# Optimization experiments

Hardware: AMD Instinct MI355X
Metric: run time of the kernel (lower is better)

The kernel has to match this reference:

```python
import jax, jax.numpy as jnp
import numpy as np

T, B, I, H, L, TAPE = 512, 1, 1024, 1024, 2, 30


def setup_inputs() -> dict:
    key = jax.random.key(0)
    ks = jax.random.split(key, 9)
    s = 1.0 / np.sqrt(H)  # pytorch LSTM default init scale
    u = lambda k, sh: jax.random.uniform(k, sh, jnp.float32, -s, s)
    return {
        "xs": jax.random.normal(ks[0], (T, B, I), jnp.float32),
        "w_ih": u(ks[1], (L, 4 * H, I)),
        "w_hh": u(ks[2], (L, 4 * H, H)),
        "b_ih": u(ks[3], (L, 4 * H)),
        "b_hh": u(ks[4], (L, 4 * H)),
        "attn_wh": jax.random.normal(ks[5], (L, H, H), jnp.float32),
        "attn_wx": jax.random.normal(ks[6], (L, H, I), jnp.float32),
        "attn_wht": jax.random.normal(ks[7], (L, H, H), jnp.float32),
        "attn_v": jax.random.normal(ks[8], (L, H), jnp.float32),
    }


def _lstm_step(x, h_prev, c_prev, w_ih, w_hh, b_ih, b_hh):
    # x: (B, I); h_prev, c_prev: (L, B, H). PyTorch gate order i,f,g,o. No dropout (eval/deterministic).
    inp = x
    hs, cs = [], []
    for l in range(L):
        g = inp @ w_ih[l].T + b_ih[l] + h_prev[l] @ w_hh[l].T + b_hh[l]
        i_g, f_g, g_g, o_g = jnp.split(g, 4, axis=-1)
        c = jax.nn.sigmoid(f_g) * c_prev[l] + jax.nn.sigmoid(i_g) * jnp.tanh(g_g)
        h = jax.nn.sigmoid(o_g) * jnp.tanh(c)
        hs.append(h)
        cs.append(c)
        inp = h
    return jnp.stack(hs), jnp.stack(cs)  # (L, B, H) each


def _forward(xs, w_ih, w_hh, b_ih, b_hh, attn_wh, attn_wx, attn_wht, attn_v):
    zeros_state = jnp.zeros((L, B, H), xs.dtype)

    # Phase 1: prev_hidden/cell tapes are never updated in the first loop, so each of the
    # first TAPE steps runs the LSTM from a zero state -> fully parallel via vmap.
    p1 = lambda x: _lstm_step(x, zeros_state, zeros_state, w_ih, w_hh, b_ih, b_hh)
    h1, c1 = jax.vmap(p1)(xs[:TAPE])  # (TAPE, L, B, H)
    h_tape = jax.lax.stop_gradient(h1)  # .detach() in the original
    c_tape = jax.lax.stop_gradient(c1)

    cum = jnp.zeros((T, H), xs.dtype)
    cum = cum.at[:TAPE].set(h1[:, -1, 0, :])  # hidden_state[-1].squeeze(), B==1

    # einsum('jll,...') / einsum('ijj,...') only use the diagonals of attn_wh / attn_wht
    diag_wh = jnp.diagonal(attn_wh, axis1=1, axis2=2)    # (L, H)
    diag_wht = jnp.diagonal(attn_wht, axis1=1, axis2=2)  # (L, H)

    def step(carry, x):
        h_tape, c_tape, prev_h = carry
        hidden_attn = diag_wh[None, :, None, :] * h_tape          # (TAPE, L, B, H)
        x_attn = jnp.einsum('lhi,bi->lbh', attn_wx, x)            # (L, B, H)
        ht_attn = diag_wht[:, None, :] * prev_h                   # (L, B, H)
        a = jnp.tanh(hidden_attn + (x_attn + ht_attn)[None])      # (TAPE, L, B, H)
        scores = jnp.einsum('tlbh,lh->tlb', a, attn_v)            # (TAPE, L, B)
        alpha = jax.nn.softmax(scores, axis=0)                    # softmax over tape dim
        new_h = jnp.einsum('tlb,tlbh->lbh', alpha, h_tape)
        new_c = jnp.einsum('tlb,tlbh->lbh', alpha, c_tape)
        h, c = _lstm_step(x, new_h, new_c, w_ih, w_hh, b_ih, b_hh)
        h_tape = jnp.concatenate([h_tape[1:], h[None]], axis=0)   # tape shift
        c_tape = jnp.concatenate([c_tape[1:], c[None]], axis=0)
        return (h_tape, c_tape, new_h), h[-1, 0, :]

    _, ys = jax.lax.scan(step, (h_tape, c_tape, zeros_state), xs[TAPE:])
    # second loop indexes cum from 0, overwriting the phase-1 entries (faithful to source)
    cum = cum.at[: T - TAPE].set(ys)
    return cum


def reference(xs, w_ih, w_hh, b_ih, b_hh, attn_wh, attn_wx, attn_wht, attn_v):
    return _forward(xs, w_ih, w_hh, b_ih, b_hh, attn_wh, attn_wx, attn_wht, attn_v)
```

## Files before the change

kernel.cpp:

```cpp
#include <hip/hip_runtime.h>
#include <math.h>

#define LSTRIDE 4194304

__device__ __forceinline__ float sigf(float x) { return 1.0f / (1.0f + expf(-x)); }

__device__ __forceinline__ float cload(const float* p) {
  return __hip_atomic_load(p, __ATOMIC_RELAXED, __HIP_MEMORY_SCOPE_AGENT);
}
__device__ __forceinline__ void cstore(float* p, float v) {
  __hip_atomic_store(p, v, __ATOMIC_RELAXED, __HIP_MEMORY_SCOPE_AGENT);
}
__device__ __forceinline__ float2 cload2(const float* p) {
  unsigned long long v = __hip_atomic_load((const unsigned long long*)p,
                                           __ATOMIC_RELAXED, __HIP_MEMORY_SCOPE_AGENT);
  float2 r;
  r.x = __uint_as_float((unsigned)v);
  r.y = __uint_as_float((unsigned)(v >> 32));
  return r;
}
__device__ __forceinline__ void cstore2(float* p, float2 v) {
  unsigned long long u = ((unsigned long long)__float_as_uint(v.y) << 32) |
                         (unsigned long long)__float_as_uint(v.x);
  __hip_atomic_store((unsigned long long*)p, u, __ATOMIC_RELAXED, __HIP_MEMORY_SCOPE_AGENT);
}

__global__ __launch_bounds__(256) void gemm_nt(
    const float* __restrict__ A, const float* __restrict__ X, float* __restrict__ Out,
    const float* __restrict__ b1, const float* __restrict__ b2,
    int M, int ldx, int ldo)
{
  __shared__ float As[64][65];
  __shared__ float Xs[64][65];
  const int tid = threadIdx.x;
  const int tn = tid & 15, tm = tid >> 4;
  const int bn = blockIdx.x * 64, bm = blockIdx.y * 64;
  float acc[4][4];
  #pragma unroll
  for (int i = 0; i < 4; ++i)
    #pragma unroll
    for (int j = 0; j < 4; ++j) acc[i][j] = 0.f;

  for (int k0 = 0; k0 < 1024; k0 += 64) {
    #pragma unroll
    for (int r = 0; r < 4; ++r) {
      int linear = r * 1024 + tid * 4;
      int nn = linear >> 6, kk = linear & 63;
      float4 av = *(const float4*)(A + (size_t)(bn + nn) * 1024 + k0 + kk);
      As[nn][kk+0] = av.x; As[nn][kk+1] = av.y; As[nn][kk+2] = av.z; As[nn][kk+3] = av.w;
      float4 xv = make_float4(0.f, 0.f, 0.f, 0.f);
      if (bm + nn < M) xv = *(const float4*)(X + (size_t)(bm + nn) * ldx + k0 + kk);
      Xs[nn][kk+0] = xv.x; Xs[nn][kk+1] = xv.y; Xs[nn][kk+2] = xv.z; Xs[nn][kk+3] = xv.w;
    }
    __syncthreads();
    #pragma unroll 16
    for (int kk = 0; kk < 64; ++kk) {
      float av[4], xv[4];
      #pragma unroll
      for (int u = 0; u < 4; ++u) { av[u] = As[tn*4+u][kk]; xv[u] = Xs[tm*4+u][kk]; }
      #pragma unroll
      for (int i = 0; i < 4; ++i)
        #pragma unroll
        for (int j = 0; j < 4; ++j) acc[i][j] += xv[i] * av[j];
    }
    __syncthreads();
  }
  #pragma unroll
  for (int i = 0; i < 4; ++i) {
    int m = bm + tm * 4 + i;
    if (m >= M) continue;
    #pragma unroll
    for (int j = 0; j < 4; ++j) {
      int n = bn + tn * 4 + j;
      float r = acc[i][j];
      if (b1) r += b1[n];
      if (b2) r += b2[n];
      Out[(size_t)m * ldo + n] = r;
    }
  }
}

__global__ void diag_k(const float* __restrict__ wh, const float* __restrict__ wht,
                       float* __restrict__ diag)
{
  int i = blockIdx.x * 256 + threadIdx.x;
  if (i < 2048) {
    int l = i >> 10, h = i & 1023;
    size_t idx = (size_t)l * 1048576 + (size_t)h * 1025;
    diag[i]        = wh[idx];
    diag[2048 + i] = wht[idx];
  }
}

__global__ __launch_bounds__(256) void phase1_l0_k(const float* __restrict__ XI0,
    float* __restrict__ tapeh, float* __restrict__ tapec, float* __restrict__ h0p1)
{
  int t = blockIdx.x;
  #pragma unroll
  for (int r = 0; r < 4; ++r) {
    int c = threadIdx.x + r * 256;
    float gi = XI0[t*4096 + c];
    float gg = XI0[t*4096 + 2048 + c];
    float go = XI0[t*4096 + 3072 + c];
    float cc = sigf(gi) * tanhf(gg);
    float hh = sigf(go) * tanhf(cc);
    tapeh[t*2048 + c] = hh;
    tapec[t*2048 + c] = cc;
    h0p1[t*1024 + c] = hh;
  }
}

__global__ __launch_bounds__(256) void phase1_l1_k(const float* __restrict__ G1,
    float* __restrict__ tapeh, float* __restrict__ tapec)
{
  int t = blockIdx.x;
  #pragma unroll
  for (int r = 0; r < 4; ++r) {
    int c = threadIdx.x + r * 256;
    float gi = G1[t*4096 + c];
    float gg = G1[t*4096 + 2048 + c];
    float go = G1[t*4096 + 3072 + c];
    float cc = sigf(gi) * tanhf(gg);
    float hh = sigf(go) * tanhf(cc);
    tapeh[t*2048 + 1024 + c] = hh;
    tapec[t*2048 + 1024 + c] = cc;
  }
}

__device__ __forceinline__ float red16(float p) {
  #pragma unroll
  for (int o = 8; o >= 1; o >>= 1) p += __shfl_xor(p, o, 16);
  return p;
}

__device__ __forceinline__ void arrive(unsigned* __restrict__ base, int gw) {
  asm volatile("s_waitcnt vmcnt(0)" ::: "memory");
  __syncthreads();
  if (threadIdx.x == 0) {
    unsigned o = __hip_atomic_fetch_add(&base[(gw >> 3) * 16], 1u,
                                        __ATOMIC_RELAXED, __HIP_MEMORY_SCOPE_AGENT);
    if (((o + 1) & 7u) == 0u) {
      unsigned o2 = __hip_atomic_fetch_add(&base[256], 1u,
                                           __ATOMIC_RELAXED, __HIP_MEMORY_SCOPE_AGENT);
      if (((o2 + 1) & 15u) == 0u)
        __hip_atomic_store(&base[320], (o2 + 1) >> 4,
                           __ATOMIC_RELAXED, __HIP_MEMORY_SCOPE_AGENT);
    }
  }
}

__device__ __forceinline__ void waitf(const unsigned* __restrict__ fOwn, unsigned tOwn,
                                      const unsigned* __restrict__ fOth, unsigned tOth) {
  if (threadIdx.x < 2) {
    const unsigned* fp = threadIdx.x ? fOth : fOwn;
    unsigned tgt = threadIdx.x ? tOth : tOwn;
    if (tgt) {
      while (__hip_atomic_load(fp, __ATOMIC_RELAXED, __HIP_MEMORY_SCOPE_AGENT) < tgt)
        __builtin_amdgcn_s_sleep(1);
    }
  }
  __syncthreads();
  asm volatile("" ::: "memory");
}

template <int LW>
__device__ __forceinline__ void run_group(
    const int gw,
    const float* __restrict__ wih, const float* __restrict__ whh,
    const float* __restrict__ bih, const float* __restrict__ bhh,
    const float* __restrict__ diag, const float* __restrict__ av,
    const float* __restrict__ XI0, const float* __restrict__ XA,
    const float* __restrict__ tapehG, const float* __restrict__ tapecG,
    const float* __restrict__ Pg,
    float* __restrict__ scoresG, float* __restrict__ prevh,
    float* __restrict__ h0cur, float* __restrict__ h1cur,
    float* __restrict__ outp, unsigned* __restrict__ bar,
    float* tape, float* hA, float* hB, float* Pl, float* tc,
    float* sc, float* aw, float* gls, float* ihs, float* ncs,
    float* bsum, float* sred)
{
  const int tid = threadIdx.x;
  const int rid = tid >> 4, sub = tid & 15;
  const int cell = (gw << 3) + (rid & 7);
  const int row = ((rid >> 3) << 10) + cell;
  const bool isScore = (gw < 29);
  const int h2 = tid * 2;

  unsigned* __restrict__ barOwn = bar + (LW ? 512 : 0);
  const unsigned* __restrict__ fOwn = barOwn + 320;
  const unsigned* __restrict__ fOth = bar + (LW ? 0 : 512) + 320;

  float wA[64];
  float wB[LW ? 64 : 1];
  {
    const float* pa = whh + (size_t)LW * LSTRIDE + (size_t)row * 1024 + sub * 64;
    #pragma unroll
    for (int i = 0; i < 16; ++i) {
      float4 v = ((const float4*)pa)[i];
      wA[4*i] = v.x; wA[4*i+1] = v.y; wA[4*i+2] = v.z; wA[4*i+3] = v.w;
    }
    if (LW) {
      const float* pb = wih + LSTRIDE + (size_t)row * 1024 + sub * 64;
      #pragma unroll
      for (int i = 0; i < 16; ++i) {
        float4 v = ((const float4*)pb)[i];
        wB[4*i] = v.x; wB[4*i+1] = v.y; wB[4*i+2] = v.z; wB[4*i+3] = v.w;
      }
    }
  }
  if (LW && sub == 0) bsum[rid] = bih[4096 + row] + bhh[4096 + row];
  for (int k = tid; k < 960; k += 512) {
    int s = k >> 5, r = k & 31;
    int rr = ((r >> 3) << 10) + (gw << 3) + (r & 7);
    Pl[s * 34 + r] = Pg[s * 4096 + rr];
  }
  for (int k = tid; k < 240; k += 512) {
    int s = k >> 3, c = k & 7;
    tc[s * 9 + c] = tapecG[s * 2048 + LW * 1024 + (gw << 3) + c];
  }
  if (isScore) {
    for (int k = tid; k < 7680; k += 512) {
      int s = k >> 8, off = (k & 255) << 2;
      *(float4*)&tape[s * 1024 + off] =
          *(const float4*)&tapehG[s * 2048 + LW * 1024 + off];
    }
  }
  const float ddx = diag[LW*1024 + h2],        ddy = diag[LW*1024 + h2 + 1];
  const float ttx = diag[2048 + LW*1024 + h2], tty = diag[2048 + LW*1024 + h2 + 1];
  const float vvx = av[LW*1024 + h2],          vvy = av[LW*1024 + h2 + 1];
  __syncthreads();

  if (isScore) {
    for (int s = gw; s < 30; s += 29) {
      float2 xa = *(const float2*)&XA[(size_t)30 * 2048 + LW * 1024 + h2];
      float part = vvx * tanhf(ddx * tape[s*1024 + h2] + xa.x)
                 + vvy * tanhf(ddy * tape[s*1024 + h2 + 1] + xa.y);
      #pragma unroll
      for (int o = 32; o >= 1; o >>= 1) part += __shfl_xor(part, o, 64);
      if ((tid & 63) == 0) sred[tid >> 6] = part;
      __syncthreads();
      if (tid == 0) {
        float tot = 0.f;
        #pragma unroll
        for (int i = 0; i < 8; ++i) tot += sred[i];
        cstore(&scoresG[LW * 32 + s], tot);
      }
      __syncthreads();
    }
  }
  arrive(barOwn, gw);

  for (int t = 30; t < 512; ++t) {
    unsigned tOwn = (unsigned)(t - 29);
    unsigned tOth;
    if (LW == 0) tOth = (t >= 33) ? (unsigned)(t - 32) : 0u;
    else         tOth = (unsigned)(t - 28);
    waitf(fOwn, tOwn, fOth, tOth);

    const int tmod = t % 30;
    const int pslot = (tmod == 0) ? 29 : tmod - 1;

    if (tid < 30) sc[tid] = cload(&scoresG[(t & 1) * 64 + LW * 32 + tid]);
    float2 hva, hvb = make_float2(0.f, 0.f), ph = make_float2(0.f, 0.f),
           xan = make_float2(0.f, 0.f);
    if (LW == 0) {
      hva = cload2(&h0cur[(size_t)((t - 1) & 3) * 1024 + h2]);
    } else {
      hva = cload2(&h0cur[(size_t)(t & 3) * 1024 + h2]);
      hvb = cload2(&h1cur[((t - 1) & 1) * 1024 + h2]);
    }
    if (t > 30) {
      ph  = cload2(&prevh[((t - 1) & 1) * 2048 + LW * 1024 + h2]);
      xan = *(const float2*)&XA[(size_t)t * 2048 + LW * 1024 + h2];
    }
    float xi = 0.f;
    if (LW == 0 && sub == 0) xi = XI0[(size_t)t * 4096 + row];
    {
      int o = (h2 >> 6) * 66 + (h2 & 63);
      hA[o] = hva.x; hA[o + 1] = hva.y;
      if (LW) { hB[o] = hvb.x; hB[o + 1] = hvb.y; }
    }
    __syncthreads();

    if (t > 30) {
      float2 hn = LW ? hvb : hva;
      float np = vvx * tanhf(ddx * hn.x + xan.x + ttx * ph.x)
               + vvy * tanhf(ddy * hn.y + xan.y + tty * ph.y);
      #pragma unroll
      for (int o = 32; o >= 1; o >>= 1) np += __shfl_xor(np, o, 64);
      if ((tid & 63) == 0) sred[tid >> 6] = np;
      const float* hbufP = LW ? hB : hA;
      float pc = 0.f;
      #pragma unroll
      for (int i = 0; i < 64; ++i) pc += wA[i] * hbufP[sub * 66 + i];
      pc = red16(pc);
      if (sub == 0) Pl[pslot * 34 + rid] = pc;
      if (isScore) {
        tape[pslot * 1024 + h2]     = hn.x;
        tape[pslot * 1024 + h2 + 1] = hn.y;
      }
    }
    if (LW) {
      float ih = 0.f;
      #pragma unroll
      for (int i = 0; i < 64; ++i) ih += wB[i] * hA[sub * 66 + i];
      ih = red16(ih);
      if (sub == 0) ihs[rid] = ih + bsum[rid];
    }
    __syncthreads();

    if (tid < 32) {
      float npv = 0.f;
      if (t > 30) {
        float x = (tid < 8) ? sred[tid] : 0.f;
        #pragma unroll
        for (int o = 4; o >= 1; o >>= 1) x += __shfl_xor(x, o, 8);
        npv = __shfl(x, 0, 32);
      }
      float v = (tid < 30) ? sc[tid] : -1e30f;
      if (t > 30 && tid == pslot) v = npv;
      float m = v;
      #pragma unroll
      for (int o = 16; o >= 1; o >>= 1) m = fmaxf(m, __shfl_xor(m, o, 32));
      float e = (tid < 30) ? expf(v - m) : 0.f;
      float sm = e;
      #pragma unroll
      for (int o = 16; o >= 1; o >>= 1) sm += __shfl_xor(sm, o, 32);
      aw[tid] = e / sm;
    }
    __syncthreads();

    {
      float p = aw[sub] * Pl[sub * 34 + rid];
      if (sub < 14) p += aw[sub + 16] * Pl[(sub + 16) * 34 + rid];
      p = red16(p);
      if (sub == 0) gls[rid] = p + (LW ? ihs[rid] : xi);
      if (rid < 8) {
        float pn = aw[sub] * tc[sub * 9 + rid];
        if (sub < 14) pn += aw[sub + 16] * tc[(sub + 16) * 9 + rid];
        pn = red16(pn);
        if (sub == 0) ncs[rid] = pn;
      }
    }
    __syncthreads();

    if (tid < 8) {
      float gi = gls[tid], gf = gls[8 + tid], gg = gls[16 + tid], go = gls[24 + tid];
      float cv = sigf(gf) * ncs[tid] + sigf(gi) * tanhf(gg);
      float hv = sigf(go) * tanhf(cv);
      if (LW == 0) {
        cstore(&h0cur[(size_t)(t & 3) * 1024 + (gw << 3) + tid], hv);
      } else {
        outp[(size_t)(t - 30) * 1024 + (gw << 3) + tid] = hv;
        cstore(&h1cur[(t & 1) * 1024 + (gw << 3) + tid], hv);
      }
      tc[tmod * 9 + tid] = cv;
    }

    if (isScore && t < 511) {
      int ss = tmod + 1 + gw; if (ss >= 30) ss -= 30;
      float ax = 0.f, ay = 0.f;
      #pragma unroll
      for (int s = 0; s < 30; ++s) {
        float as = aw[s];
        ax += as * tape[s * 1024 + h2];
        ay += as * tape[s * 1024 + h2 + 1];
      }
      if (gw == 0) cstore2(&prevh[(t & 1) * 2048 + LW * 1024 + h2],
                           make_float2(ax, ay));
      float2 xa2 = *(const float2*)&XA[(size_t)(t + 1) * 2048 + LW * 1024 + h2];
      float part = vvx * tanhf(ddx * tape[ss * 1024 + h2] + xa2.x + ttx * ax)
                 + vvy * tanhf(ddy * tape[ss * 1024 + h2 + 1] + xa2.y + tty * ay);
      #pragma unroll
      for (int o = 32; o >= 1; o >>= 1) part += __shfl_xor(part, o, 64);
      if ((tid & 63) == 0) sred[tid >> 6] = part;
      __syncthreads();
      if (tid == 0) {
        float tot = 0.f;
        #pragma unroll
        for (int i = 0; i < 8; ++i) tot += sred[i];
        cstore(&scoresG[((t + 1) & 1) * 64 + LW * 32 + ss], tot);
      }
    }

    arrive(barOwn, gw);
  }
}

__global__ __launch_bounds__(512, 2) void scan_fused(
    const float* __restrict__ wih, const float* __restrict__ whh,
    const float* __restrict__ bih, const float* __restrict__ bhh,
    const float* __restrict__ diag, const float* __restrict__ av,
    const float* __restrict__ XI0, const float* __restrict__ XA,
    const float* __restrict__ tapehG, const float* __restrict__ tapecG,
    const float* __restrict__ P0g, const float* __restrict__ P1g,
    float* __restrict__ scoresG, float* __restrict__ prevh,
    float* __restrict__ h0cur, float* __restrict__ h1cur,
    float* __restrict__ outp, unsigned* __restrict__ bar)
{
  __shared__ float tape[30 * 1024];
  __shared__ float hA[16 * 66], hB[16 * 66];
  __shared__ float Pl[30 * 34];
  __shared__ float tc[30 * 9];
  __shared__ float sc[32], aw[32], gls[32], ihs[32], ncs[8], bsum[32], sred[8];
  if (blockIdx.x < 128)
    run_group<0>(blockIdx.x, wih, whh, bih, bhh, diag, av, XI0, XA, tapehG, tapecG,
                 P0g, scoresG, prevh, h0cur, h1cur, outp, bar,
                 tape, hA, hB, Pl, tc, sc, aw, gls, ihs, ncs, bsum, sred);
  else
    run_group<1>(blockIdx.x - 128, wih, whh, bih, bhh, diag, av, XI0, XA, tapehG, tapecG,
                 P1g, scoresG, prevh, h0cur, h1cur, outp, bar,
                 tape, hA, hB, Pl, tc, sc, aw, gls, ihs, ncs, bsum, sred);
}

extern "C" void kernel_launch(void* const* d_in, const int* in_sizes, int n_in,
                              void* d_out, int out_size, void* d_ws, size_t ws_size,
                              hipStream_t stream) {
  (void)in_sizes; (void)n_in; (void)out_size; (void)ws_size;
  const float* xs    = (const float*)d_in[0];
  const float* w_ih  = (const float*)d_in[1];
  const float* w_hh  = (const float*)d_in[2];
  const float* b_ih  = (const float*)d_in[3];
  const float* b_hh  = (const float*)d_in[4];
  const float* a_wh  = (const float*)d_in[5];
  const float* a_wx  = (const float*)d_in[6];
  const float* a_wht = (const float*)d_in[7];
  const float* a_v   = (const float*)d_in[8];
  float* outp = (float*)d_out;

  float* ws     = (float*)d_ws;
  float* XI0    = ws;
  float* XA     = XI0    + 512 * 4096;
  float* tapehG = XA     + 512 * 2048;
  float* tapecG = tapehG + 30 * 2048;
  float* P0g    = tapecG + 30 * 2048;
  float* P1g    = P0g    + 30 * 4096;
  float* diag   = P1g    + 30 * 4096;
  float* scor   = diag   + 4096;
  float* prevh  = scor   + 128;
  float* h0cur  = prevh  + 4096;
  float* h1cur  = h0cur  + 4096;
  float* h0p1   = h1cur  + 2048;
  float* G1b    = h0p1   + 30 * 1024;
  unsigned* bar = (unsigned*)(G1b + 30 * 4096);

  hipMemsetAsync(outp + (size_t)482 * 1024, 0, 30 * 1024 * sizeof(float), stream);
  hipMemsetAsync(bar, 0, 4096, stream);

  diag_k<<<8, 256, 0, stream>>>(a_wh, a_wht, diag);

  gemm_nt<<<dim3(64, 8), 256, 0, stream>>>(w_ih, xs, XI0, b_ih, b_hh, 512, 1024, 4096);
  gemm_nt<<<dim3(16, 8), 256, 0, stream>>>(a_wx, xs, XA, nullptr, nullptr, 512, 1024, 2048);
  gemm_nt<<<dim3(16, 8), 256, 0, stream>>>(a_wx + LSTRIDE / 4, xs, XA + 1024, nullptr, nullptr, 512, 1024, 2048);

  phase1_l0_k<<<30, 256, 0, stream>>>(XI0, tapehG, tapecG, h0p1);
  gemm_nt<<<dim3(64, 1), 256, 0, stream>>>(w_ih + LSTRIDE, h0p1, G1b, b_ih + 4096, b_hh + 4096, 30, 1024, 4096);
  phase1_l1_k<<<30, 256, 0, stream>>>(G1b, tapehG, tapecG);

  gemm_nt<<<dim3(64, 1), 256, 0, stream>>>(w_hh, tapehG, P0g, nullptr, nullptr, 30, 2048, 4096);
  gemm_nt<<<dim3(64, 1), 256, 0, stream>>>(w_hh + LSTRIDE, tapehG + 1024, P1g, nullptr, nullptr, 30, 2048, 4096);

  const float* wihp = w_ih;
  const float* whhp = w_hh;
  const float* bihp = b_ih;
  const float* bhhp = b_hh;
  void* kargs[] = {
    (void*)&wihp, (void*)&whhp, (void*)&bihp, (void*)&bhhp,
    (void*)&diag, (void*)&a_v,  (void*)&XI0,  (void*)&XA,
    (void*)&tapehG, (void*)&tapecG, (void*)&P0g, (void*)&P1g,
    (void*)&scor, (void*)&prevh, (void*)&h0cur, (void*)&h1cur,
    (void*)&outp, (void*)&bar
  };
  hipLaunchCooperativeKernel((void*)scan_fused, dim3(256), dim3(512), kargs, 0, stream);
}
```

Baseline: 3.821 ms.

## Compute attention scores redundantly per block to drop global score exchange

Each workgroup now keeps the full tape, diagonal weights and prev-hidden in LDS and computes all 30 attention scores locally after every step. This removes the global scoresG/prevh buffers and the extra dependency on other groups' score writes. The barrier becomes a flatter two-level counter with cumulative targets, and it is signalled earlier, before the attention reduction. Exact tanh, sigmoid, exp and division are swapped for fast intrinsic approximations. The trade-off is redundant per-block work, more LDS use per block, and lower numeric accuracy.

```diff
diff --git a/kernel.cpp b/kernel.cpp
--- a/kernel.cpp
+++ b/kernel.cpp
@@ -3,7 +3,14 @@
 
 #define LSTRIDE 4194304
 
-__device__ __forceinline__ float sigf(float x) { return 1.0f / (1.0f + expf(-x)); }
+__device__ __forceinline__ float fast_tanh(float x) {
+  x = fminf(9.f, fmaxf(-9.f, x));
+  float e = __expf(2.f * x);
+  return (e - 1.f) * __builtin_amdgcn_rcpf(e + 1.f);
+}
+__device__ __forceinline__ float sigf(float x) {
+  return __builtin_amdgcn_rcpf(1.f + __expf(-x));
+}
 
 __device__ __forceinline__ float cload(const float* p) {
   return __hip_atomic_load(p, __ATOMIC_RELAXED, __HIP_MEMORY_SCOPE_AGENT);
@@ -18,11 +25,6 @@
   r.x = __uint_as_float((unsigned)v);
   r.y = __uint_as_float((unsigned)(v >> 32));
   return r;
-}
-__device__ __forceinline__ void cstore2(float* p, float2 v) {
-  unsigned long long u = ((unsigned long long)__float_as_uint(v.y) << 32) |
-                         (unsigned long long)__float_as_uint(v.x);
-  __hip_atomic_store((unsigned long long*)p, u, __ATOMIC_RELAXED, __HIP_MEMORY_SCOPE_AGENT);
 }
 
 __global__ __launch_bounds__(256) void gemm_nt(
@@ -137,15 +139,11 @@
   asm volatile("s_waitcnt vmcnt(0)" ::: "memory");
   __syncthreads();
   if (threadIdx.x == 0) {
-    unsigned o = __hip_atomic_fetch_add(&base[(gw >> 3) * 16], 1u,
+    unsigned o = __hip_atomic_fetch_add(&base[(gw >> 4) * 16], 1u,
                                         __ATOMIC_RELAXED, __HIP_MEMORY_SCOPE_AGENT);
-    if (((o + 1) & 7u) == 0u) {
-      unsigned o2 = __hip_atomic_fetch_add(&base[256], 1u,
-                                           __ATOMIC_RELAXED, __HIP_MEMORY_SCOPE_AGENT);
-      if (((o2 + 1) & 15u) == 0u)
-        __hip_atomic_store(&base[320], (o2 + 1) >> 4,
-                           __ATOMIC_RELAXED, __HIP_MEMORY_SCOPE_AGENT);
-    }
+    if (((o + 1) & 15u) == 0u)
+      __hip_atomic_fetch_add(&base[128], 1u,
+                             __ATOMIC_RELAXED, __HIP_MEMORY_SCOPE_AGENT);
   }
 }
 
@@ -161,6 +159,31 @@
   }
   __syncthreads();
   asm volatile("" ::: "memory");
+}
+
+__device__ __forceinline__ void fast_scores(
+    const float* __restrict__ XAt, int skip, int tid,
+    const float* tape, const float* pvh,
+    const float* ddl, const float* ttl, const float* vvl, float* sc)
+{
+  const int w = tid >> 6, l = tid & 63;
+  #pragma unroll 1
+  for (int s = w; s < 30; s += 8) {
+    if (s == skip) continue;
+    float acc = 0.f;
+    #pragma unroll 4
+    for (int k = 0; k < 8; ++k) {
+      const int d = l * 2 + k * 128;
+      float2 tv = *(const float2*)&tape[s * 1024 + d];
+      float2 xa = *(const float2*)&XAt[d];
+      float2 pv = *(const float2*)&pvh[d];
+      acc += vvl[d]     * fast_tanh(ddl[d]     * tv.x + xa.x + ttl[d]     * pv.x)
+           + vvl[d + 1] * fast_tanh(ddl[d + 1] * tv.y + xa.y + ttl[d + 1] * pv.y);
+    }
+    #pragma unroll
+    for (int o = 32; o >= 1; o >>= 1) acc += __shfl_xor(acc, o, 64);
+    if (l == 0) sc[s] = acc;
+  }
 }
 
 template <int LW>
@@ -172,23 +195,21 @@
     const float* __restrict__ XI0, const float* __restrict__ XA,
     const float* __restrict__ tapehG, const float* __restrict__ tapecG,
     const float* __restrict__ Pg,
-    float* __restrict__ scoresG, float* __restrict__ prevh,
     float* __restrict__ h0cur, float* __restrict__ h1cur,
     float* __restrict__ outp, unsigned* __restrict__ bar,
-    float* tape, float* hA, float* hB, float* Pl, float* tc,
+    float* tape, float* ddl, float* ttl, float* vvl, float* pvh,
+    float* hA, float* hB, float* Pl, float* tc,
     float* sc, float* aw, float* gls, float* ihs, float* ncs,
     float* bsum, float* sred)
 {
   const int tid = threadIdx.x;
   const int rid = tid >> 4, sub = tid & 15;
-  const int cell = (gw << 3) + (rid & 7);
-  const int row = ((rid >> 3) << 10) + cell;
-  const bool isScore = (gw < 29);
+  const int row = ((rid >> 3) << 10) + (gw << 3) + (rid & 7);
   const int h2 = tid * 2;
 
-  unsigned* __restrict__ barOwn = bar + (LW ? 512 : 0);
-  const unsigned* __restrict__ fOwn = barOwn + 320;
-  const unsigned* __restrict__ fOth = bar + (LW ? 0 : 512) + 320;
+  unsigned* __restrict__ barOwn = bar + (LW ? 256 : 0);
+  const unsigned* __restrict__ fOwn = barOwn + 128;
+  const unsigned* __restrict__ fOth = bar + (LW ? 0 : 256) + 128;
 
   float wA[64];
   float wB[LW ? 64 : 1];
@@ -218,87 +239,68 @@
     int s = k >> 3, c = k & 7;
     tc[s * 9 + c] = tapecG[s * 2048 + LW * 1024 + (gw << 3) + c];
   }
-  if (isScore) {
-    for (int k = tid; k < 7680; k += 512) {
-      int s = k >> 8, off = (k & 255) << 2;
-      *(float4*)&tape[s * 1024 + off] =
-          *(const float4*)&tapehG[s * 2048 + LW * 1024 + off];
-    }
-  }
-  const float ddx = diag[LW*1024 + h2],        ddy = diag[LW*1024 + h2 + 1];
-  const float ttx = diag[2048 + LW*1024 + h2], tty = diag[2048 + LW*1024 + h2 + 1];
-  const float vvx = av[LW*1024 + h2],          vvy = av[LW*1024 + h2 + 1];
+  for (int k = tid; k < 7680; k += 512) {
+    int s = k >> 8, off = (k & 255) << 2;
+    *(float4*)&tape[s * 1024 + off] =
+        *(const float4*)&tapehG[s * 2048 + LW * 1024 + off];
+  }
+  {
+    float2 d0 = *(const float2*)&diag[LW * 1024 + h2];
+    float2 t0 = *(const float2*)&diag[2048 + LW * 1024 + h2];
+    float2 v0 = *(const float2*)&av[LW * 1024 + h2];
+    ddl[h2] = d0.x; ddl[h2+1] = d0.y;
+    ttl[h2] = t0.x; ttl[h2+1] = t0.y;
+    vvl[h2] = v0.x; vvl[h2+1] = v0.y;
+    pvh[h2] = 0.f;  pvh[h2+1] = 0.f;
+  }
   __syncthreads();
 
-  if (isScore) {
-    for (int s = gw; s < 30; s += 29) {
-      float2 xa = *(const float2*)&XA[(size_t)30 * 2048 + LW * 1024 + h2];
-      float part = vvx * tanhf(ddx * tape[s*1024 + h2] + xa.x)
-                 + vvy * tanhf(ddy * tape[s*1024 + h2 + 1] + xa.y);
-      #pragma unroll
-      for (int o = 32; o >= 1; o >>= 1) part += __shfl_xor(part, o, 64);
-      if ((tid & 63) == 0) sred[tid >> 6] = part;
-      __syncthreads();
-      if (tid == 0) {
-        float tot = 0.f;
-        #pragma unroll
-        for (int i = 0; i < 8; ++i) tot += sred[i];
-        cstore(&scoresG[LW * 32 + s], tot);
-      }
-      __syncthreads();
-    }
-  }
-  arrive(barOwn, gw);
+  fast_scores(XA + (size_t)30 * 2048 + LW * 1024, -1, tid,
+              tape, pvh, ddl, ttl, vvl, sc);
+  float xi = 0.f;
+  if (LW == 0 && sub == 0) xi = XI0[(size_t)30 * 4096 + row];
+  float2 xan = make_float2(0.f, 0.f);
+  float pvx = 0.f, pvy = 0.f;
 
   for (int t = 30; t < 512; ++t) {
-    unsigned tOwn = (unsigned)(t - 29);
+    unsigned tOwn = (t > 30) ? 8u * (unsigned)(t - 30) : 0u;
     unsigned tOth;
-    if (LW == 0) tOth = (t >= 33) ? (unsigned)(t - 32) : 0u;
-    else         tOth = (unsigned)(t - 28);
+    if (LW == 0) tOth = (t > 33) ? 8u * (unsigned)(t - 33) : 0u;
+    else         tOth = 8u * (unsigned)(t - 29);
     waitf(fOwn, tOwn, fOth, tOth);
 
     const int tmod = t % 30;
     const int pslot = (tmod == 0) ? 29 : tmod - 1;
 
-    if (tid < 30) sc[tid] = cload(&scoresG[(t & 1) * 64 + LW * 32 + tid]);
-    float2 hva, hvb = make_float2(0.f, 0.f), ph = make_float2(0.f, 0.f),
-           xan = make_float2(0.f, 0.f);
+    float2 hva = make_float2(0.f, 0.f), hvb = make_float2(0.f, 0.f);
     if (LW == 0) {
-      hva = cload2(&h0cur[(size_t)((t - 1) & 3) * 1024 + h2]);
+      if (t > 30) hva = cload2(&h0cur[(size_t)((t - 1) & 3) * 1024 + h2]);
     } else {
       hva = cload2(&h0cur[(size_t)(t & 3) * 1024 + h2]);
-      hvb = cload2(&h1cur[((t - 1) & 1) * 1024 + h2]);
-    }
-    if (t > 30) {
-      ph  = cload2(&prevh[((t - 1) & 1) * 2048 + LW * 1024 + h2]);
-      xan = *(const float2*)&XA[(size_t)t * 2048 + LW * 1024 + h2];
-    }
-    float xi = 0.f;
-    if (LW == 0 && sub == 0) xi = XI0[(size_t)t * 4096 + row];
+      if (t > 30) hvb = cload2(&h1cur[((t - 1) & 1) * 1024 + h2]);
+    }
     {
       int o = (h2 >> 6) * 66 + (h2 & 63);
-      hA[o] = hva.x; hA[o + 1] = hva.y;
-      if (LW) { hB[o] = hvb.x; hB[o + 1] = hvb.y; }
+      if (LW || t > 30) { hA[o] = hva.x; hA[o + 1] = hva.y; }
+      if (LW && t > 30) { hB[o] = hvb.x; hB[o + 1] = hvb.y; }
     }
     __syncthreads();
 
     if (t > 30) {
       float2 hn = LW ? hvb : hva;
-      float np = vvx * tanhf(ddx * hn.x + xan.x + ttx * ph.x)
-               + vvy * tanhf(ddy * hn.y + xan.y + tty * ph.y);
+      float np = vvl[h2]     * fast_tanh(ddl[h2]     * hn.x + xan.x + ttl[h2]     * pvx)
+               + vvl[h2 + 1] * fast_tanh(ddl[h2 + 1] * hn.y + xan.y + ttl[h2 + 1] * pvy);
       #pragma unroll
       for (int o = 32; o >= 1; o >>= 1) np += __shfl_xor(np, o, 64);
       if ((tid & 63) == 0) sred[tid >> 6] = np;
-      const float* hbufP = LW ? hB : hA;
+      tape[pslot * 1024 + h2]     = hn.x;
+      tape[pslot * 1024 + h2 + 1] = hn.y;
+      const float* hp = LW ? hB : hA;
       float pc = 0.f;
       #pragma unroll
-      for (int i = 0; i < 64; ++i) pc += wA[i] * hbufP[sub * 66 + i];
+      for (int i = 0; i < 64; ++i) pc += wA[i] * hp[sub * 66 + i];
       pc = red16(pc);
       if (sub == 0) Pl[pslot * 34 + rid] = pc;
-      if (isScore) {
-        tape[pslot * 1024 + h2]     = hn.x;
-        tape[pslot * 1024 + h2 + 1] = hn.y;
-      }
     }
     if (LW) {
       float ih = 0.f;
@@ -322,11 +324,11 @@
       float m = v;
       #pragma unroll
       for (int o = 16; o >= 1; o >>= 1) m = fmaxf(m, __shfl_xor(m, o, 32));
-      float e = (tid < 30) ? expf(v - m) : 0.f;
+      float e = (tid < 30) ? __expf(v - m) : 0.f;
       float sm = e;
       #pragma unroll
       for (int o = 16; o >= 1; o >>= 1) sm += __shfl_xor(sm, o, 32);
-      aw[tid] = e / sm;
+      aw[tid] = e * __builtin_amdgcn_rcpf(sm);
     }
     __syncthreads();
 
@@ -346,8 +348,8 @@
 
     if (tid < 8) {
       float gi = gls[tid], gf = gls[8 + tid], gg = gls[16 + tid], go = gls[24 + tid];
-      float cv = sigf(gf) * ncs[tid] + sigf(gi) * tanhf(gg);
-      float hv = sigf(go) * tanhf(cv);
+      float cv = sigf(gf) * ncs[tid] + sigf(gi) * fast_tanh(gg);
+      float hv = sigf(go) * fast_tanh(cv);
       if (LW == 0) {
         cstore(&h0cur[(size_t)(t & 3) * 1024 + (gw << 3) + tid], hv);
       } else {
@@ -357,33 +359,24 @@
       tc[tmod * 9 + tid] = cv;
     }
 
-    if (isScore && t < 511) {
-      int ss = tmod + 1 + gw; if (ss >= 30) ss -= 30;
+    arrive(barOwn, gw);
+
+    if (t < 511) {
       float ax = 0.f, ay = 0.f;
-      #pragma unroll
+      #pragma unroll 1
       for (int s = 0; s < 30; ++s) {
-        float as = aw[s];
-        ax += as * tape[s * 1024 + h2];
-        ay += as * tape[s * 1024 + h2 + 1];
+        float a = aw[s];
+        float2 tv = *(const float2*)&tape[s * 1024 + h2];
+        ax += a * tv.x; ay += a * tv.y;
       }
-      if (gw == 0) cstore2(&prevh[(t & 1) * 2048 + LW * 1024 + h2],
-                           make_float2(ax, ay));
-      float2 xa2 = *(const float2*)&XA[(size_t)(t + 1) * 2048 + LW * 1024 + h2];
-      float part = vvx * tanhf(ddx * tape[ss * 1024 + h2] + xa2.x + ttx * ax)
-                 + vvy * tanhf(ddy * tape[ss * 1024 + h2 + 1] + xa2.y + tty * ay);
-      #pragma unroll
-      for (int o = 32; o >= 1; o >>= 1) part += __shfl_xor(part, o, 64);
-      if ((tid & 63) == 0) sred[tid >> 6] = part;
+      pvh[h2] = ax; pvh[h2 + 1] = ay;
+      pvx = ax; pvy = ay;
       __syncthreads();
-      if (tid == 0) {
-        float tot = 0.f;
-        #pragma unroll
-        for (int i = 0; i < 8; ++i) tot += sred[i];
-        cstore(&scoresG[((t + 1) & 1) * 64 + LW * 32 + ss], tot);
-      }
-    }
-
-    arrive(barOwn, gw);
+      fast_scores(XA + (size_t)(t + 1) * 2048 + LW * 1024, tmod, tid,
+                  tape, pvh, ddl, ttl, vvl, sc);
+      xan = *(const float2*)&XA[(size_t)(t + 1) * 2048 + LW * 1024 + h2];
+      if (LW == 0 && sub == 0) xi = XI0[(size_t)(t + 1) * 4096 + row];
+    }
   }
 }
 
@@ -394,23 +387,25 @@
     const float* __restrict__ XI0, const float* __restrict__ XA,
     const float* __restrict__ tapehG, const float* __restrict__ tapecG,
     const float* __restrict__ P0g, const float* __restrict__ P1g,
-    float* __restrict__ scoresG, float* __restrict__ prevh,
     float* __restrict__ h0cur, float* __restrict__ h1cur,
     float* __restrict__ outp, unsigned* __restrict__ bar)
 {
   __shared__ float tape[30 * 1024];
+  __shared__ float ddl[1024], ttl[1024], vvl[1024], pvh[1024];
   __shared__ float hA[16 * 66], hB[16 * 66];
   __shared__ float Pl[30 * 34];
   __shared__ float tc[30 * 9];
   __shared__ float sc[32], aw[32], gls[32], ihs[32], ncs[8], bsum[32], sred[8];
   if (blockIdx.x < 128)
     run_group<0>(blockIdx.x, wih, whh, bih, bhh, diag, av, XI0, XA, tapehG, tapecG,
-                 P0g, scoresG, prevh, h0cur, h1cur, outp, bar,
-                 tape, hA, hB, Pl, tc, sc, aw, gls, ihs, ncs, bsum, sred);
+                 P0g, h0cur, h1cur, outp, bar,
+                 tape, ddl, ttl, vvl, pvh, hA, hB, Pl, tc,
+                 sc, aw, gls, ihs, ncs, bsum, sred);
   else
     run_group<1>(blockIdx.x - 128, wih, whh, bih, bhh, diag, av, XI0, XA, tapehG, tapecG,
-                 P1g, scoresG, prevh, h0cur, h1cur, outp, bar,
-                 tape, hA, hB, Pl, tc, sc, aw, gls, ihs, ncs, bsum, sred);
+                 P1g, h0cur, h1cur, outp, bar,
+                 tape, ddl, ttl, vvl, pvh, hA, hB, Pl, tc,
+                 sc, aw, gls, ihs, ncs, bsum, sred);
 }
 
 extern "C" void kernel_launch(void* const* d_in, const int* in_sizes, int n_in,
@@ -436,16 +431,14 @@
   float* P0g    = tapecG + 30 * 2048;
   float* P1g    = P0g    + 30 * 4096;
   float* diag   = P1g    + 30 * 4096;
-  float* scor   = diag   + 4096;
-  float* prevh  = scor   + 128;
-  float* h0cur  = prevh  + 4096;
+  float* h0cur  = diag   + 4096;
   float* h1cur  = h0cur  + 4096;
   float* h0p1   = h1cur  + 2048;
   float* G1b    = h0p1   + 30 * 1024;
   unsigned* bar = (unsigned*)(G1b + 30 * 4096);
 
   hipMemsetAsync(outp + (size_t)482 * 1024, 0, 30 * 1024 * sizeof(float), stream);
-  hipMemsetAsync(bar, 0, 4096, stream);
+  hipMemsetAsync(bar, 0, 2048, stream);
 
   diag_k<<<8, 256, 0, stream>>>(a_wh, a_wht, diag);
 
@@ -468,8 +461,7 @@
     (void*)&wihp, (void*)&whhp, (void*)&bihp, (void*)&bhhp,
     (void*)&diag, (void*)&a_v,  (void*)&XI0,  (void*)&XA,
     (void*)&tapehG, (void*)&tapecG, (void*)&P0g, (void*)&P1g,
-    (void*)&scor, (void*)&prevh, (void*)&h0cur, (void*)&h1cur,
-    (void*)&outp, (void*)&bar
+    (void*)&h0cur, (void*)&h1cur, (void*)&outp, (void*)&bar
   };
   hipLaunchCooperativeKernel((void*)scan_fused, dim3(256), dim3(512), kargs, 0, stream);
 }
```

Result: slower. 5.465 ms (+43.0%).

## Split tape score work across half-blocks, flatten barrier, use fast transcendentals

Applied to the files above, without the earlier changes.

Each pair of blocks now shares one tape slot, each holding half the hidden dimension, so per-block shared tape and score work are halved and 58 blocks compute partial scores that are summed at softmax time. The two-level barrier becomes a single-level counter with targets scaled by 8. Global loads of XA and XI0 are hoisted ahead of the barrier wait. Sigmoid, tanh, exp and division in the recurrent path switch to fast approximate intrinsics, which may slightly change numerics.

```diff
diff --git a/kernel.cpp b/kernel.cpp
--- a/kernel.cpp
+++ b/kernel.cpp
@@ -3,7 +3,15 @@
 
 #define LSTRIDE 4194304
 
-__device__ __forceinline__ float sigf(float x) { return 1.0f / (1.0f + expf(-x)); }
+__device__ __forceinline__ float fast_tanh(float x) {
+  x = fminf(9.f, fmaxf(-9.f, x));
+  float e = __expf(2.f * x);
+  return (e - 1.f) * __builtin_amdgcn_rcpf(e + 1.f);
+}
+__device__ __forceinline__ float fsig(float x) {
+  return __builtin_amdgcn_rcpf(1.f + __expf(-x));
+}
+__device__ __forceinline__ float sigp(float x) { return 1.0f / (1.0f + expf(-x)); }
 
 __device__ __forceinline__ float cload(const float* p) {
   return __hip_atomic_load(p, __ATOMIC_RELAXED, __HIP_MEMORY_SCOPE_AGENT);
@@ -18,11 +26,6 @@
   r.x = __uint_as_float((unsigned)v);
   r.y = __uint_as_float((unsigned)(v >> 32));
   return r;
-}
-__device__ __forceinline__ void cstore2(float* p, float2 v) {
-  unsigned long long u = ((unsigned long long)__float_as_uint(v.y) << 32) |
-                         (unsigned long long)__float_as_uint(v.x);
-  __hip_atomic_store((unsigned long long*)p, u, __ATOMIC_RELAXED, __HIP_MEMORY_SCOPE_AGENT);
 }
 
 __global__ __launch_bounds__(256) void gemm_nt(
@@ -102,8 +105,8 @@
     float gi = XI0[t*4096 + c];
     float gg = XI0[t*4096 + 2048 + c];
     float go = XI0[t*4096 + 3072 + c];
-    float cc = sigf(gi) * tanhf(gg);
-    float hh = sigf(go) * tanhf(cc);
+    float cc = sigp(gi) * tanhf(gg);
+    float hh = sigp(go) * tanhf(cc);
     tapeh[t*2048 + c] = hh;
     tapec[t*2048 + c] = cc;
     h0p1[t*1024 + c] = hh;
@@ -120,8 +123,8 @@
     float gi = G1[t*4096 + c];
     float gg = G1[t*4096 + 2048 + c];
     float go = G1[t*4096 + 3072 + c];
-    float cc = sigf(gi) * tanhf(gg);
-    float hh = sigf(go) * tanhf(cc);
+    float cc = sigp(gi) * tanhf(gg);
+    float hh = sigp(go) * tanhf(cc);
     tapeh[t*2048 + 1024 + c] = hh;
     tapec[t*2048 + 1024 + c] = cc;
   }
@@ -137,15 +140,11 @@
   asm volatile("s_waitcnt vmcnt(0)" ::: "memory");
   __syncthreads();
   if (threadIdx.x == 0) {
-    unsigned o = __hip_atomic_fetch_add(&base[(gw >> 3) * 16], 1u,
+    unsigned o = __hip_atomic_fetch_add(&base[(gw >> 4) * 16], 1u,
                                         __ATOMIC_RELAXED, __HIP_MEMORY_SCOPE_AGENT);
-    if (((o + 1) & 7u) == 0u) {
-      unsigned o2 = __hip_atomic_fetch_add(&base[256], 1u,
-                                           __ATOMIC_RELAXED, __HIP_MEMORY_SCOPE_AGENT);
-      if (((o2 + 1) & 15u) == 0u)
-        __hip_atomic_store(&base[320], (o2 + 1) >> 4,
-                           __ATOMIC_RELAXED, __HIP_MEMORY_SCOPE_AGENT);
-    }
+    if (((o + 1) & 15u) == 0u)
+      __hip_atomic_fetch_add(&base[128], 1u,
+                             __ATOMIC_RELAXED, __HIP_MEMORY_SCOPE_AGENT);
   }
 }
 
@@ -176,19 +175,20 @@
     float* __restrict__ h0cur, float* __restrict__ h1cur,
     float* __restrict__ outp, unsigned* __restrict__ bar,
     float* tape, float* hA, float* hB, float* Pl, float* tc,
-    float* sc, float* aw, float* gls, float* ihs, float* ncs,
+    float* sc2, float* aw, float* gls, float* ihs, float* ncs,
     float* bsum, float* sred)
 {
   const int tid = threadIdx.x;
   const int rid = tid >> 4, sub = tid & 15;
-  const int cell = (gw << 3) + (rid & 7);
-  const int row = ((rid >> 3) << 10) + cell;
-  const bool isScore = (gw < 29);
+  const int row = ((rid >> 3) << 10) + (gw << 3) + (rid & 7);
+  const bool isScore = (gw < 58);
+  const int ii = gw >> 1, half = gw & 1;
+  const int d = (half << 9) + tid;
   const int h2 = tid * 2;
 
-  unsigned* __restrict__ barOwn = bar + (LW ? 512 : 0);
-  const unsigned* __restrict__ fOwn = barOwn + 320;
-  const unsigned* __restrict__ fOth = bar + (LW ? 0 : 512) + 320;
+  unsigned* __restrict__ barOwn = bar + (LW ? 256 : 0);
+  const unsigned* __restrict__ fOwn = barOwn + 128;
+  const unsigned* __restrict__ fOth = bar + (LW ? 0 : 256) + 128;
 
   float wA[64];
   float wB[LW ? 64 : 1];
@@ -219,22 +219,24 @@
     tc[s * 9 + c] = tapecG[s * 2048 + LW * 1024 + (gw << 3) + c];
   }
   if (isScore) {
-    for (int k = tid; k < 7680; k += 512) {
-      int s = k >> 8, off = (k & 255) << 2;
-      *(float4*)&tape[s * 1024 + off] =
-          *(const float4*)&tapehG[s * 2048 + LW * 1024 + off];
+    for (int k = tid; k < 3840; k += 512) {
+      int s = k >> 7, off = (k & 127) << 2;
+      *(float4*)&tape[s * 512 + off] =
+          *(const float4*)&tapehG[s * 2048 + LW * 1024 + (half << 9) + off];
     }
   }
   const float ddx = diag[LW*1024 + h2],        ddy = diag[LW*1024 + h2 + 1];
   const float ttx = diag[2048 + LW*1024 + h2], tty = diag[2048 + LW*1024 + h2 + 1];
   const float vvx = av[LW*1024 + h2],          vvy = av[LW*1024 + h2 + 1];
+  const float ddT = diag[LW*1024 + d];
+  const float ttT = diag[2048 + LW*1024 + d];
+  const float vvT = av[LW*1024 + d];
   __syncthreads();
 
   if (isScore) {
-    for (int s = gw; s < 30; s += 29) {
-      float2 xa = *(const float2*)&XA[(size_t)30 * 2048 + LW * 1024 + h2];
-      float part = vvx * tanhf(ddx * tape[s*1024 + h2] + xa.x)
-                 + vvy * tanhf(ddy * tape[s*1024 + h2 + 1] + xa.y);
+    for (int s = ii; s < 30; s += 29) {
+      float xa = XA[(size_t)30 * 2048 + LW * 1024 + d];
+      float part = vvT * fast_tanh(ddT * tape[s * 512 + tid] + xa);
       #pragma unroll
       for (int o = 32; o >= 1; o >>= 1) part += __shfl_xor(part, o, 64);
       if ((tid & 63) == 0) sred[tid >> 6] = part;
@@ -243,7 +245,7 @@
         float tot = 0.f;
         #pragma unroll
         for (int i = 0; i < 8; ++i) tot += sred[i];
-        cstore(&scoresG[LW * 32 + s], tot);
+        cstore(&scoresG[LW * 64 + s * 2 + half], tot);
       }
       __syncthreads();
     }
@@ -251,54 +253,61 @@
   arrive(barOwn, gw);
 
   for (int t = 30; t < 512; ++t) {
-    unsigned tOwn = (unsigned)(t - 29);
+    float2 xan = make_float2(0.f, 0.f);
+    if (t > 30) xan = *(const float2*)&XA[(size_t)t * 2048 + LW * 1024 + h2];
+    float xi = 0.f;
+    if (LW == 0 && sub == 0) xi = XI0[(size_t)t * 4096 + row];
+    float xaT = 0.f;
+    if (isScore && t < 511) xaT = XA[(size_t)(t + 1) * 2048 + LW * 1024 + d];
+
+    unsigned tOwn = 8u * (unsigned)(t - 29);
     unsigned tOth;
-    if (LW == 0) tOth = (t >= 33) ? (unsigned)(t - 32) : 0u;
-    else         tOth = (unsigned)(t - 28);
+    if (LW == 0)
+      tOth = (t >= 34) ? 8u * (unsigned)(t - 32) : 0u;
+    else
+      tOth = 8u * (unsigned)(t - 28);
     waitf(fOwn, tOwn, fOth, tOth);
 
     const int tmod = t % 30;
     const int pslot = (tmod == 0) ? 29 : tmod - 1;
 
-    if (tid < 30) sc[tid] = cload(&scoresG[(t & 1) * 64 + LW * 32 + tid]);
-    float2 hva, hvb = make_float2(0.f, 0.f), ph = make_float2(0.f, 0.f),
-           xan = make_float2(0.f, 0.f);
+    if (tid < 60) sc2[tid] = cload(&scoresG[(t & 1) * 128 + LW * 64 + tid]);
+    float2 hva = make_float2(0.f, 0.f), hvb = make_float2(0.f, 0.f),
+           ph = make_float2(0.f, 0.f);
     if (LW == 0) {
-      hva = cload2(&h0cur[(size_t)((t - 1) & 3) * 1024 + h2]);
+      if (t > 30) hva = cload2(&h0cur[(size_t)((t - 1) & 3) * 1024 + h2]);
     } else {
       hva = cload2(&h0cur[(size_t)(t & 3) * 1024 + h2]);
-      hvb = cload2(&h1cur[((t - 1) & 1) * 1024 + h2]);
-    }
-    if (t > 30) {
-      ph  = cload2(&prevh[((t - 1) & 1) * 2048 + LW * 1024 + h2]);
-      xan = *(const float2*)&XA[(size_t)t * 2048 + LW * 1024 + h2];
-    }
-    float xi = 0.f;
-    if (LW == 0 && sub == 0) xi = XI0[(size_t)t * 4096 + row];
+      if (t > 30) hvb = cload2(&h1cur[((t - 1) & 1) * 1024 + h2]);
+    }
+    if (t > 30) ph = cload2(&prevh[((t - 1) & 1) * 2048 + LW * 1024 + h2]);
     {
       int o = (h2 >> 6) * 66 + (h2 & 63);
-      hA[o] = hva.x; hA[o + 1] = hva.y;
-      if (LW) { hB[o] = hvb.x; hB[o + 1] = hvb.y; }
+      if (LW || t > 30) { hA[o] = hva.x; hA[o + 1] = hva.y; }
+      if (LW && t > 30) { hB[o] = hvb.x; hB[o + 1] = hvb.y; }
     }
     __syncthreads();
 
     if (t > 30) {
       float2 hn = LW ? hvb : hva;
-      float np = vvx * tanhf(ddx * hn.x + xan.x + ttx * ph.x)
-               + vvy * tanhf(ddy * hn.y + xan.y + tty * ph.y);
+      float np = vvx * fast_tanh(ddx * hn.x + xan.x + ttx * ph.x)
+               + vvy * fast_tanh(ddy * hn.y + xan.y + tty * ph.y);
       #pragma unroll
       for (int o = 32; o >= 1; o >>= 1) np += __shfl_xor(np, o, 64);
       if ((tid & 63) == 0) sred[tid >> 6] = np;
-      const float* hbufP = LW ? hB : hA;
+      if (isScore) {
+        int loc = h2 - (half << 9);
+        if ((unsigned)loc < 512u) {
+          tape[pslot * 512 + loc]     = hn.x;
+          tape[pslot * 512 + loc + 1] = hn.y;
+        }
+      }
+      const float* hp = LW ? hB : hA;
       float pc = 0.f;
       #pragma unroll
-      for (int i = 0; i < 64; ++i) pc += wA[i] * hbufP[sub * 66 + i];
+      for (int i = 0; i < 64; ++i) pc += wA[i] * hp[sub * 66 + i];
       pc = red16(pc);
       if (sub == 0) Pl[pslot * 34 + rid] = pc;
-      if (isScore) {
-        tape[pslot * 1024 + h2]     = hn.x;
-        tape[pslot * 1024 + h2 + 1] = hn.y;
-      }
     }
     if (LW) {
       float ih = 0.f;
@@ -317,16 +326,16 @@
         for (int o = 4; o >= 1; o >>= 1) x += __shfl_xor(x, o, 8);
         npv = __shfl(x, 0, 32);
       }
-      float v = (tid < 30) ? sc[tid] : -1e30f;
+      float v = (tid < 30) ? sc2[2 * tid] + sc2[2 * tid + 1] : -1e30f;
       if (t > 30 && tid == pslot) v = npv;
       float m = v;
       #pragma unroll
       for (int o = 16; o >= 1; o >>= 1) m = fmaxf(m, __shfl_xor(m, o, 32));
-      float e = (tid < 30) ? expf(v - m) : 0.f;
+      float e = (tid < 30) ? __expf(v - m) : 0.f;
       float sm = e;
       #pragma unroll
       for (int o = 16; o >= 1; o >>= 1) sm += __shfl_xor(sm, o, 32);
-      aw[tid] = e / sm;
+      aw[tid] = e * __builtin_amdgcn_rcpf(sm);
     }
     __syncthreads();
 
@@ -346,8 +355,8 @@
 
     if (tid < 8) {
       float gi = gls[tid], gf = gls[8 + tid], gg = gls[16 + tid], go = gls[24 + tid];
-      float cv = sigf(gf) * ncs[tid] + sigf(gi) * tanhf(gg);
-      float hv = sigf(go) * tanhf(cv);
+      float cv = fsig(gf) * ncs[tid] + fsig(gi) * fast_tanh(gg);
+      float hv = fsig(go) * fast_tanh(cv);
       if (LW == 0) {
         cstore(&h0cur[(size_t)(t & 3) * 1024 + (gw << 3) + tid], hv);
       } else {
@@ -358,19 +367,12 @@
     }
 
     if (isScore && t < 511) {
-      int ss = tmod + 1 + gw; if (ss >= 30) ss -= 30;
-      float ax = 0.f, ay = 0.f;
-      #pragma unroll
-      for (int s = 0; s < 30; ++s) {
-        float as = aw[s];
-        ax += as * tape[s * 1024 + h2];
-        ay += as * tape[s * 1024 + h2 + 1];
-      }
-      if (gw == 0) cstore2(&prevh[(t & 1) * 2048 + LW * 1024 + h2],
-                           make_float2(ax, ay));
-      float2 xa2 = *(const float2*)&XA[(size_t)(t + 1) * 2048 + LW * 1024 + h2];
-      float part = vvx * tanhf(ddx * tape[ss * 1024 + h2] + xa2.x + ttx * ax)
-                 + vvy * tanhf(ddy * tape[ss * 1024 + h2 + 1] + xa2.y + tty * ay);
+      int ss = tmod + 1 + ii; if (ss >= 30) ss -= 30;
+      float acc = 0.f;
+      #pragma unroll
+      for (int s = 0; s < 30; ++s) acc += aw[s] * tape[s * 512 + tid];
+      if (ii == 0) cstore(&prevh[(t & 1) * 2048 + LW * 1024 + d], acc);
+      float part = vvT * fast_tanh(ddT * tape[ss * 512 + tid] + xaT + ttT * acc);
       #pragma unroll
       for (int o = 32; o >= 1; o >>= 1) part += __shfl_xor(part, o, 64);
       if ((tid & 63) == 0) sred[tid >> 6] = part;
@@ -379,7 +381,7 @@
         float tot = 0.f;
         #pragma unroll
         for (int i = 0; i < 8; ++i) tot += sred[i];
-        cstore(&scoresG[((t + 1) & 1) * 64 + LW * 32 + ss], tot);
+        cstore(&scoresG[((t + 1) & 1) * 128 + LW * 64 + ss * 2 + half], tot);
       }
     }
 
@@ -398,19 +400,19 @@
     float* __restrict__ h0cur, float* __restrict__ h1cur,
     float* __restrict__ outp, unsigned* __restrict__ bar)
 {
-  __shared__ float tape[30 * 1024];
+  __shared__ float tape[30 * 512];
   __shared__ float hA[16 * 66], hB[16 * 66];
   __shared__ float Pl[30 * 34];
   __shared__ float tc[30 * 9];
-  __shared__ float sc[32], aw[32], gls[32], ihs[32], ncs[8], bsum[32], sred[8];
+  __shared__ float sc2[64], aw[32], gls[32], ihs[32], ncs[8], bsum[32], sred[8];
   if (blockIdx.x < 128)
     run_group<0>(blockIdx.x, wih, whh, bih, bhh, diag, av, XI0, XA, tapehG, tapecG,
                  P0g, scoresG, prevh, h0cur, h1cur, outp, bar,
-                 tape, hA, hB, Pl, tc, sc, aw, gls, ihs, ncs, bsum, sred);
+                 tape, hA, hB, Pl, tc, sc2, aw, gls, ihs, ncs, bsum, sred);
   else
     run_group<1>(blockIdx.x - 128, wih, whh, bih, bhh, diag, av, XI0, XA, tapehG, tapecG,
                  P1g, scoresG, prevh, h0cur, h1cur, outp, bar,
-                 tape, hA, hB, Pl, tc, sc, aw, gls, ihs, ncs, bsum, sred);
+                 tape, hA, hB, Pl, tc, sc2, aw, gls, ihs, ncs, bsum, sred);
 }
 
 extern "C" void kernel_launch(void* const* d_in, const int* in_sizes, int n_in,
@@ -437,7 +439,7 @@
   float* P1g    = P0g    + 30 * 4096;
   float* diag   = P1g    + 30 * 4096;
   float* scor   = diag   + 4096;
-  float* prevh  = scor   + 128;
+  float* prevh  = scor   + 256;
   float* h0cur  = prevh  + 4096;
   float* h1cur  = h0cur  + 4096;
   float* h0p1   = h1cur  + 2048;
@@ -445,7 +447,7 @@
   unsigned* bar = (unsigned*)(G1b + 30 * 4096);
 
   hipMemsetAsync(outp + (size_t)482 * 1024, 0, 30 * 1024 * sizeof(float), stream);
-  hipMemsetAsync(bar, 0, 4096, stream);
+  hipMemsetAsync(bar, 0, 2048, stream);
 
   diag_k<<<8, 256, 0, stream>>>(a_wh, a_wht, diag);
 
```

Result: faster. 3.543 ms (-7.3%).
